# Kernel tuning notes

Measured on AMD Instinct MI355X. Metric: run time of the kernel, lower is better.

Reference implementation:

```python
import jax, jax.numpy as jnp
import numpy as np

N, T, F, H = 64, 256, 1024, 1024

def setup_inputs() -> dict:
    key = jax.random.key(0)
    k1, k2 = jax.random.split(key)
    x = jax.random.normal(k1, (N, T, F), dtype=jnp.float32)
    # xavier-normal: std = sqrt(2 / (fan_in + fan_out))
    std = np.sqrt(2.0 / ((F + H) + 4 * H)).astype(np.float32)
    weight = jax.random.normal(k2, (F + H, 4 * H), dtype=jnp.float32) * std
    bias = jnp.zeros((1, 4 * H), dtype=jnp.float32)
    return {"x": x, "weight": weight, "bias": bias}


def reference(x, weight, bias):
    # x: [N, T, F]; weight: [F+H, 4H]; bias: [1, 4H]
    n, t, f = x.shape
    h_dim = weight.shape[1] // 4

    def step(carry, xt):
        h, mem = carry  # [N, H] each
        xh = jnp.concatenate([xt, h], axis=-1)          # [N, F+H]
        a = xh @ weight + bias                          # [N, 4H]
        i, fg, o, g = jnp.split(a, 4, axis=-1)
        mem = jax.nn.sigmoid(fg) * mem + jax.nn.sigmoid(i) * jnp.tanh(g)
        h = jax.nn.sigmoid(o) * jnp.tanh(mem)
        return (h, mem), h

    h0 = jnp.zeros((n, h_dim), dtype=x.dtype)
    m0 = jnp.zeros((n, h_dim), dtype=x.dtype)
    (h, mem), z_tnh = jax.lax.scan(step, (h0, m0), jnp.swapaxes(x, 0, 1))
    z = jnp.swapaxes(z_tnh, 0, 1)                       # [N, T, H]
    return z, h, mem
```

## Files before the change

### kernel.cpp

```cpp
#include <hip/hip_runtime.h>

typedef unsigned short u16;
typedef unsigned int   u32;
typedef __attribute__((ext_vector_type(8))) short bf16x8;
typedef __attribute__((ext_vector_type(4))) float f32x4;

#define NB 64
#define TT 256
#define FF 1024
#define HH 1024
#define KK 2048
#define GG 4096
#define NBLK 256

#define WPACK_SZ  (KK*GG)
#define XPACK_SZ  ((size_t)NB*TT*FF)
#define HPACK_SZ  (2*4*32*64*8)
#define FLAGS_SZ  (4*64*4)

__device__ __forceinline__ u16 f2bf(float f) {
  u32 u = __float_as_uint(f);
  u32 r = (u + 0x7FFFu + ((u >> 16) & 1u)) >> 16;
  return (u16)r;
}

__global__ void pack_w(const float* __restrict__ W, u16* __restrict__ wp) {
  int tid = blockIdx.x * blockDim.x + threadIdx.x;
  if (tid >= (KK * GG / 16)) return;
  int j  = tid & 7;
  int g  = (tid >> 3) & 3;
  int kt = (tid >> 5) & 63;
  int ct = tid >> 11;
  int k  = kt * 32 + g * 8 + j;
  const float* src = W + (size_t)k * GG + ct * 16;
  u16* dst = wp + (size_t)(ct * 64 + kt) * 512 + j;
  float4 v0 = *(const float4*)(src + 0);
  float4 v1 = *(const float4*)(src + 4);
  float4 v2 = *(const float4*)(src + 8);
  float4 v3 = *(const float4*)(src + 12);
  float vv[16] = {v0.x,v0.y,v0.z,v0.w, v1.x,v1.y,v1.z,v1.w,
                  v2.x,v2.y,v2.z,v2.w, v3.x,v3.y,v3.z,v3.w};
  #pragma unroll
  for (int c = 0; c < 16; ++c) dst[(size_t)(g * 16 + c) * 8] = f2bf(vv[c]);
}

__global__ void pack_x(const float* __restrict__ X, u16* __restrict__ xp) {
  int tid = blockIdx.x * blockDim.x + threadIdx.x;
  if (tid >= (int)(NB * TT * FF / 8)) return;
  int l  = tid & 63;
  int kt = (tid >> 6) & 31;
  int rt = (tid >> 11) & 3;
  int t  = tid >> 13;
  int n  = rt * 16 + (l & 15);
  int f  = kt * 32 + (l >> 4) * 8;
  const float* src = X + (size_t)n * TT * FF + (size_t)t * FF + f;
  float4 a = *(const float4*)(src);
  float4 b = *(const float4*)(src + 4);
  u16 tmp[8] = { f2bf(a.x), f2bf(a.y), f2bf(a.z), f2bf(a.w),
                 f2bf(b.x), f2bf(b.y), f2bf(b.z), f2bf(b.w) };
  *(uint4*)(xp + (size_t)((t * 4 + rt) * 32 + kt) * 512 + l * 8) = *(uint4*)tmp;
}

__global__ void init_state(u32* __restrict__ flags) {
  int tid = threadIdx.x;
  #pragma unroll
  for (int i = 0; i < 4; ++i)
    __hip_atomic_store(&flags[i * 256 + tid], 0u, __ATOMIC_RELAXED,
                       __HIP_MEMORY_SCOPE_AGENT);
}

__launch_bounds__(1024, 1)
__global__ void lstm_main(const u16* __restrict__ wp, const u16* __restrict__ xp,
                          u32* __restrict__ hp32, const float* __restrict__ bias,
                          float* __restrict__ z, float* __restrict__ hout,
                          float* __restrict__ memout, u32* flags) {
  const int b   = blockIdx.x;
  const int cgi = b & 63;
  const int rt  = b >> 6;
  const int tid = threadIdx.x;
  const int w16 = tid >> 6;
  const int g   = w16 & 3;
  const int s   = w16 >> 2;
  const int l   = tid & 63;
  const int ct  = g * 64 + cgi;

  const u16* bp = wp + (size_t)ct * 32768 + l * 8;
  const float bv = (s == 0) ? bias[ct * 16 + (l & 15)] : 0.f;
  u32* gf = flags + rt * 256;

  __shared__ __align__(16) u16 whl[57344];
  __shared__ u32   hs32[8192];
  __shared__ float gl[4][4][16][16];

  #pragma unroll
  for (int j = 0; j < 7; ++j) {
    int byte = tid * 16 + j * 16384;
    int f    = byte >> 10;
    int ll   = (byte & 1023) >> 4;
    int gg   = f / 28;
    int kt   = f % 28 + 4;
    const u16* src = wp + (size_t)(gg * 64 + cgi) * 32768
                        + (size_t)(32 + kt) * 512 + ll * 8;
    *(uint4*)((char*)whl + byte) = *(const uint4*)src;
  }
  __syncthreads();

  const int er  = tid >> 4;
  const int ec  = tid & 15;
  const int m   = rt * 16 + er;
  const int col = cgi * 16 + ec;
  const int col0 = col & ~1;
  const int kt2  = col0 >> 5;
  const int g2   = (col0 >> 3) & 3;
  const int l2   = er | (g2 << 4);
  const int cbase = kt2 * 256 + l2 * 4 + ((col0 & 7) >> 1);

  float memv = 0.0f;

  for (int t = 0; t < TT; ++t) {
    const int p = t & 1;
    const u16* ax = xp + (size_t)((t * 4 + rt) * 32 + s * 8) * 512 + l * 8;
    const u16* bx = bp + (size_t)(s * 8) * 512;

    f32x4 acc0 = {bv, bv, bv, bv};
    f32x4 acc1 = {0.f, 0.f, 0.f, 0.f};
    #pragma unroll
    for (int kt = 0; kt < 8; kt += 2) {
      bf16x8 a0 = *(const bf16x8*)(ax + (size_t)kt * 512);
      bf16x8 b0 = *(const bf16x8*)(bx + (size_t)kt * 512);
      bf16x8 a1 = *(const bf16x8*)(ax + (size_t)(kt + 1) * 512);
      bf16x8 b1 = *(const bf16x8*)(bx + (size_t)(kt + 1) * 512);
      acc0 = __builtin_amdgcn_mfma_f32_16x16x32_bf16(a0, b0, acc0, 0, 0, 0);
      acc1 = __builtin_amdgcn_mfma_f32_16x16x32_bf16(a1, b1, acc1, 0, 0, 0);
    }

    if (t != 0) {
      const u32 tgt = (u32)t;
      const int fc  = w16 * 4 + (l & 3);
      for (;;) {
        u32 v = __hip_atomic_load(&gf[fc * 4], __ATOMIC_RELAXED,
                                  __HIP_MEMORY_SCOPE_AGENT);
        if (fc == cgi) v = tgt;
        if (!__any((int)(v < tgt))) break;
        __builtin_amdgcn_s_sleep(1);
      }
      const u32* hsrc = hp32 + (size_t)(p * 4 + rt) * 8192 + w16 * 512;
      u32 tmpv[8];
      #pragma unroll
      for (int i = 0; i < 8; ++i)
        tmpv[i] = __hip_atomic_load(hsrc + i * 64 + l, __ATOMIC_RELAXED,
                                    __HIP_MEMORY_SCOPE_AGENT);
      #pragma unroll
      for (int i = 0; i < 8; ++i)
        hs32[w16 * 512 + i * 64 + l] = tmpv[i];
      __syncthreads();

      const char* hb = (const char*)hs32;
      {
        bf16x8 aL = *(const bf16x8*)(hb + (size_t)s * 1024 + l * 16);
        bf16x8 bL = *(const bf16x8*)(bp + (size_t)(32 + s) * 512);
        acc0 = __builtin_amdgcn_mfma_f32_16x16x32_bf16(aL, bL, acc0, 0, 0, 0);
      }
      const char* hb2 = hb + (size_t)(4 + 7 * s) * 1024 + l * 16;
      const u16*  bh  = whl + (size_t)(g * 28 + 7 * s) * 512 + l * 8;
      #pragma unroll
      for (int kt = 0; kt < 7; ++kt) {
        bf16x8 a0 = *(const bf16x8*)(hb2 + (size_t)kt * 1024);
        bf16x8 b0 = *(const bf16x8*)(bh + (size_t)kt * 512);
        if (kt & 1) acc0 = __builtin_amdgcn_mfma_f32_16x16x32_bf16(a0, b0, acc0, 0, 0, 0);
        else        acc1 = __builtin_amdgcn_mfma_f32_16x16x32_bf16(a0, b0, acc1, 0, 0, 0);
      }
    }

    #pragma unroll
    for (int r = 0; r < 4; ++r)
      gl[s][g][(l >> 4) * 4 + r][l & 15] = acc0[r] + acc1[r];
    __syncthreads();

    float h;
    if (tid < 256) {
      float ai = (gl[0][0][er][ec] + gl[1][0][er][ec]) +
                 (gl[2][0][er][ec] + gl[3][0][er][ec]);
      float af = (gl[0][1][er][ec] + gl[1][1][er][ec]) +
                 (gl[2][1][er][ec] + gl[3][1][er][ec]);
      float ao = (gl[0][2][er][ec] + gl[1][2][er][ec]) +
                 (gl[2][2][er][ec] + gl[3][2][er][ec]);
      float ag = (gl[0][3][er][ec] + gl[1][3][er][ec]) +
                 (gl[2][3][er][ec] + gl[3][3][er][ec]);
      float si = 1.f / (1.f + __expf(-ai));
      float sf = 1.f / (1.f + __expf(-af));
      float so = 1.f / (1.f + __expf(-ao));
      float tg = 1.f - 2.f / (__expf(2.f * ag) + 1.f);
      memv = sf * memv + si * tg;
      float th = 1.f - 2.f / (__expf(2.f * memv) + 1.f);
      h = so * th;

      float hn = __shfl_xor(h, 1);
      if ((ec & 1) == 0) {
        u32 pair = (u32)f2bf(h) | ((u32)f2bf(hn) << 16);
        __hip_atomic_store(&hp32[(size_t)((p ^ 1) * 4 + rt) * 8192 + cbase], pair,
                           __ATOMIC_RELAXED, __HIP_MEMORY_SCOPE_AGENT);
      }
    }

    if (t < TT - 1) {
      __syncthreads();
      if (tid == 0)
        __hip_atomic_store(&gf[cgi * 4], (u32)(t + 1), __ATOMIC_RELAXED,
                           __HIP_MEMORY_SCOPE_AGENT);
    }

    if (tid < 256) {
      z[((size_t)m * TT + t) * HH + col] = h;
      if (t == TT - 1) hout[(size_t)m * HH + col] = h;
    }
  }
  if (tid < 256) memout[(size_t)m * HH + col] = memv;
}

extern "C" void kernel_launch(void* const* d_in, const int* in_sizes, int n_in,
                              void* d_out, int out_size, void* d_ws, size_t ws_size,
                              hipStream_t stream) {
  const float* x    = (const float*)d_in[0];
  const float* W    = (const float*)d_in[1];
  const float* bias = (const float*)d_in[2];

  float* z      = (float*)d_out;
  float* hout   = z + (size_t)NB * TT * HH;
  float* memout = hout + (size_t)NB * HH;

  u16* wp = (u16*)d_ws;
  u16* xp = wp + WPACK_SZ;
  u16* hp = xp + XPACK_SZ;
  u32* flags = (u32*)(hp + HPACK_SZ);

  hipLaunchKernelGGL(pack_w, dim3(2048), dim3(256), 0, stream, W, wp);
  hipLaunchKernelGGL(pack_x, dim3(8192), dim3(256), 0, stream, x, xp);
  hipLaunchKernelGGL(init_state, dim3(1), dim3(256), 0, stream, flags);

  hipLaunchKernelGGL(lstm_main, dim3(NBLK), dim3(1024), 0, stream,
                     wp, xp, (u32*)hp, bias, z, hout, memout, flags);
}
```

Before: 801.0 us.

## Software-pipeline next-step input projection behind the recurrent h load

```diff
diff --git a/kernel.cpp b/kernel.cpp
--- a/kernel.cpp
+++ b/kernel.cpp
@@ -115,25 +115,29 @@
   const int l2   = er | (g2 << 4);
   const int cbase = kt2 * 256 + l2 * 4 + ((col0 & 7) >> 1);
 
+  const u16* bx = bp + (size_t)(s * 8) * 512;
+
   float memv = 0.0f;
 
-  for (int t = 0; t < TT; ++t) {
-    const int p = t & 1;
-    const u16* ax = xp + (size_t)((t * 4 + rt) * 32 + s * 8) * 512 + l * 8;
-    const u16* bx = bp + (size_t)(s * 8) * 512;
-
-    f32x4 acc0 = {bv, bv, bv, bv};
-    f32x4 acc1 = {0.f, 0.f, 0.f, 0.f};
+  f32x4 cx0 = {bv, bv, bv, bv};
+  f32x4 cx1 = {0.f, 0.f, 0.f, 0.f};
+  {
+    const u16* ax = xp + (size_t)((0 * 4 + rt) * 32 + s * 8) * 512 + l * 8;
     #pragma unroll
     for (int kt = 0; kt < 8; kt += 2) {
       bf16x8 a0 = *(const bf16x8*)(ax + (size_t)kt * 512);
       bf16x8 b0 = *(const bf16x8*)(bx + (size_t)kt * 512);
       bf16x8 a1 = *(const bf16x8*)(ax + (size_t)(kt + 1) * 512);
       bf16x8 b1 = *(const bf16x8*)(bx + (size_t)(kt + 1) * 512);
-      acc0 = __builtin_amdgcn_mfma_f32_16x16x32_bf16(a0, b0, acc0, 0, 0, 0);
-      acc1 = __builtin_amdgcn_mfma_f32_16x16x32_bf16(a1, b1, acc1, 0, 0, 0);
-    }
-
+      cx0 = __builtin_amdgcn_mfma_f32_16x16x32_bf16(a0, b0, cx0, 0, 0, 0);
+      cx1 = __builtin_amdgcn_mfma_f32_16x16x32_bf16(a1, b1, cx1, 0, 0, 0);
+    }
+  }
+
+  for (int t = 0; t < TT; ++t) {
+    const int p = t & 1;
+
+    u32 tmpv[8];
     if (t != 0) {
       const u32 tgt = (u32)t;
       const int fc  = w16 * 4 + (l & 3);
@@ -144,12 +148,31 @@
         if (!__any((int)(v < tgt))) break;
         __builtin_amdgcn_s_sleep(1);
       }
+      asm volatile("" ::: "memory");
       const u32* hsrc = hp32 + (size_t)(p * 4 + rt) * 8192 + w16 * 512;
-      u32 tmpv[8];
       #pragma unroll
       for (int i = 0; i < 8; ++i)
         tmpv[i] = __hip_atomic_load(hsrc + i * 64 + l, __ATOMIC_RELAXED,
                                     __HIP_MEMORY_SCOPE_AGENT);
+      asm volatile("" ::: "memory");
+    }
+
+    f32x4 nx0 = {bv, bv, bv, bv};
+    f32x4 nx1 = {0.f, 0.f, 0.f, 0.f};
+    if (t < TT - 1) {
+      const u16* axn = xp + (size_t)(((t + 1) * 4 + rt) * 32 + s * 8) * 512 + l * 8;
+      #pragma unroll
+      for (int kt = 0; kt < 8; kt += 2) {
+        bf16x8 a0 = *(const bf16x8*)(axn + (size_t)kt * 512);
+        bf16x8 b0 = *(const bf16x8*)(bx + (size_t)kt * 512);
+        bf16x8 a1 = *(const bf16x8*)(axn + (size_t)(kt + 1) * 512);
+        bf16x8 b1 = *(const bf16x8*)(bx + (size_t)(kt + 1) * 512);
+        nx0 = __builtin_amdgcn_mfma_f32_16x16x32_bf16(a0, b0, nx0, 0, 0, 0);
+        nx1 = __builtin_amdgcn_mfma_f32_16x16x32_bf16(a1, b1, nx1, 0, 0, 0);
+      }
+    }
+
+    if (t != 0) {
       #pragma unroll
       for (int i = 0; i < 8; ++i)
         hs32[w16 * 512 + i * 64 + l] = tmpv[i];
@@ -159,7 +182,7 @@
       {
         bf16x8 aL = *(const bf16x8*)(hb + (size_t)s * 1024 + l * 16);
         bf16x8 bL = *(const bf16x8*)(bp + (size_t)(32 + s) * 512);
-        acc0 = __builtin_amdgcn_mfma_f32_16x16x32_bf16(aL, bL, acc0, 0, 0, 0);
+        cx0 = __builtin_amdgcn_mfma_f32_16x16x32_bf16(aL, bL, cx0, 0, 0, 0);
       }
       const char* hb2 = hb + (size_t)(4 + 7 * s) * 1024 + l * 16;
       const u16*  bh  = whl + (size_t)(g * 28 + 7 * s) * 512 + l * 8;
@@ -167,14 +190,14 @@
       for (int kt = 0; kt < 7; ++kt) {
         bf16x8 a0 = *(const bf16x8*)(hb2 + (size_t)kt * 1024);
         bf16x8 b0 = *(const bf16x8*)(bh + (size_t)kt * 512);
-        if (kt & 1) acc0 = __builtin_amdgcn_mfma_f32_16x16x32_bf16(a0, b0, acc0, 0, 0, 0);
-        else        acc1 = __builtin_amdgcn_mfma_f32_16x16x32_bf16(a0, b0, acc1, 0, 0, 0);
+        if (kt & 1) cx0 = __builtin_amdgcn_mfma_f32_16x16x32_bf16(a0, b0, cx0, 0, 0, 0);
+        else        cx1 = __builtin_amdgcn_mfma_f32_16x16x32_bf16(a0, b0, cx1, 0, 0, 0);
       }
     }
 
     #pragma unroll
     for (int r = 0; r < 4; ++r)
-      gl[s][g][(l >> 4) * 4 + r][l & 15] = acc0[r] + acc1[r];
+      gl[s][g][(l >> 4) * 4 + r][l & 15] = cx0[r] + cx1[r];
     __syncthreads();
 
     float h;
@@ -204,7 +227,9 @@
     }
 
     if (t < TT - 1) {
+      asm volatile("s_waitcnt vmcnt(0)" ::: "memory");
       __syncthreads();
+      asm volatile("" ::: "memory");
       if (tid == 0)
         __hip_atomic_store(&gf[cgi * 4], (u32)(t + 1), __ATOMIC_RELAXED,
                            __HIP_MEMORY_SCOPE_AGENT);
@@ -214,6 +239,9 @@
       z[((size_t)m * TT + t) * HH + col] = h;
       if (t == TT - 1) hout[(size_t)m * HH + col] = h;
     }
+
+    cx0 = nx0;
+    cx1 = nx1;
   }
   if (tid < 256) memout[(size_t)m * HH + col] = memv;
 }
```

New measurement: 1.358 ms. +69.6%, slower.
